# Performance work log

Hardware: AMD Instinct MI355X
Metric: run time of the kernel (lower is better)

## Reference

```python
import jax, jax.numpy as jnp
import numpy as np

D_MODEL = 1024
H = 16
D_K = D_MODEL // H
B, S = 2, 2048

def setup_inputs() -> dict:
    key = jax.random.key(0)
    ks = jax.random.split(key, 13)
    scale = 1.0 / np.sqrt(D_MODEL)
    mk = lambda k: jax.random.normal(k, (D_MODEL, D_MODEL), dtype=jnp.float32) * scale
    return {
        'q': jax.random.normal(ks[0], (B, S, D_MODEL), dtype=jnp.float32),
        'k': jax.random.normal(ks[1], (B, S, D_MODEL), dtype=jnp.float32),
        'v': jax.random.normal(ks[2], (B, S, D_MODEL), dtype=jnp.float32),
        'mask': jax.random.randint(ks[3], (B, 1, S, S), 0, 2, dtype=jnp.int32),
        'wq': mk(ks[4]), 'bq': jnp.zeros((D_MODEL,), jnp.float32),
        'wk': mk(ks[5]), 'bk': jnp.zeros((D_MODEL,), jnp.float32),
        'wv': mk(ks[6]), 'bv': jnp.zeros((D_MODEL,), jnp.float32),
        'wo': mk(ks[7]), 'bo': jnp.zeros((D_MODEL,), jnp.float32),
    }

def reference(q, k, v, mask, wq, bq, wk, bk, wv, bv, wo, bo):
    b, s, _ = q.shape
    # linear projections then split heads: [B,S,D] -> [B,H,S,Dk]
    def proj(x, w, bias):
        y = x @ w + bias
        return y.reshape(b, -1, H, D_K).transpose(0, 2, 1, 3)
    Q = proj(q, wq, bq)
    K = proj(k, wk, bk)
    V = proj(v, wv, bv)
    scores = jnp.einsum('bhqd,bhkd->bhqk', Q, K) / jnp.sqrt(jnp.float32(D_K))
    # faithful to source: masked positions are set to 1e-9 (not -inf)
    scores = jnp.where(mask == 0, jnp.float32(1e-9), scores)
    attn = jax.nn.softmax(scores, axis=-1)  # dropout is identity in eval mode
    x = jnp.einsum('bhqk,bhkd->bhqd', attn, V)
    x = x.transpose(0, 2, 1, 3).reshape(b, s, D_MODEL)
    return x @ wo + bo
```

## Files before the change

### kernel.cpp

```cpp
#include <hip/hip_runtime.h>
#include <hip/hip_bf16.h>

#define DM 1024
#define HEADS 16
#define DKK 64
#define BB 2
#define SS 2048
#define MROWS (BB*SS)

typedef __attribute__((ext_vector_type(8))) short bf16x8;
typedef __attribute__((ext_vector_type(4))) float f32x4;
typedef __attribute__((ext_vector_type(2))) unsigned int uv2;
typedef __hip_bfloat16 bf16;

#define SC2 0.1803368801f
#define MB2 1.442695041e-9f

__device__ __forceinline__ void async16(const void* g, void* l) {
    __builtin_amdgcn_global_load_lds((const __attribute__((address_space(1))) void*)g,
                                     (__attribute__((address_space(3))) void*)l, 16, 0, 0);
}

__global__ void prep_kernel(const float* __restrict__ q, const float* __restrict__ k,
                            const float* __restrict__ v,
                            const float* __restrict__ wq, const float* __restrict__ wk,
                            const float* __restrict__ wv, const float* __restrict__ wo,
                            const int* __restrict__ mask,
                            bf16* __restrict__ qkv, bf16* __restrict__ wcat,
                            unsigned long long* __restrict__ bits) {
    __shared__ float tile[32][33];
    const int bid = blockIdx.x;
    const int tid = threadIdx.x;
    if (bid < 12288) {
        const int z = bid >> 12;
        const int i = ((bid & 4095) << 8) + tid;
        const float* src = z == 0 ? q : (z == 1 ? k : v);
        float4 val = ((const float4*)src)[i];
        union { bf16 b[4]; ushort4 u; } cvt;
        cvt.b[0] = __float2bfloat16(val.x);
        cvt.b[1] = __float2bfloat16(val.y);
        cvt.b[2] = __float2bfloat16(val.z);
        cvt.b[3] = __float2bfloat16(val.w);
        ((ushort4*)(qkv + (size_t)z * MROWS * DM))[i] = cvt.u;
    } else if (bid < 12288 + 4096) {
        const int t = bid - 12288;
        const int z = t >> 10;
        const int bx = t & 31, by = (t >> 5) & 31;
        const float* src = z == 0 ? wq : (z == 1 ? wk : (z == 2 ? wv : wo));
        bf16* dst = wcat + ((size_t)z << 20);
        const int tx = tid & 31, ty = tid >> 5;
        const int x = bx * 32 + tx, y0 = by * 32 + ty;
#pragma unroll
        for (int i = 0; i < 32; i += 8)
            tile[ty + i][tx] = src[(size_t)(y0 + i) * DM + x];
        __syncthreads();
        const int nx = by * 32 + tx, ny0 = bx * 32 + ty;
#pragma unroll
        for (int i = 0; i < 32; i += 8)
            dst[(size_t)(ny0 + i) * DM + nx] = __float2bfloat16(tile[tx][ty + i]);
    } else {
        const int i4 = ((bid - 16384) << 8) + tid;
        const int4 m = ((const int4*)mask)[i4];
        unsigned long long vv = (unsigned long long)(
            (m.x != 0 ? 1u : 0u) | (m.y != 0 ? 2u : 0u) |
            (m.z != 0 ? 4u : 0u) | (m.w != 0 ? 8u : 0u));
        vv <<= ((tid & 15) * 4);
        vv |= __shfl_xor(vv, 1);
        vv |= __shfl_xor(vv, 2);
        vv |= __shfl_xor(vv, 4);
        vv |= __shfl_xor(vv, 8);
        if ((tid & 15) == 0) bits[i4 >> 4] = vv;
    }
}

__global__ __launch_bounds__(256) void gemm_qkv(const bf16* __restrict__ qb, const bf16* __restrict__ kb,
                                                const bf16* __restrict__ vb, const bf16* __restrict__ wcat,
                                                const float* __restrict__ bq, const float* __restrict__ bk,
                                                const float* __restrict__ bv,
                                                bf16* __restrict__ Qh, bf16* __restrict__ Kh,
                                                bf16* __restrict__ Vt) {
    __shared__ __align__(16) bf16 lA[128 * 32];
    __shared__ __align__(16) bf16 lB[128 * 32];
    const int seg = blockIdx.x >> 3;
    const bf16* A    = seg == 0 ? qb : (seg == 1 ? kb : vb);
    const bf16* Bt   = wcat + ((size_t)seg << 20);
    const float* bias = seg == 0 ? bq : (seg == 1 ? bk : bv);

    const int tid  = threadIdx.x;
    const int lane = tid & 63;
    const int lm   = lane & 15;
    const int quad = lane >> 4;
    const int w    = tid >> 6;
    const int wm   = w >> 1, wn = w & 1;
    const int m0   = blockIdx.y * 128;
    const int n0   = (blockIdx.x & 7) * 128;
    const int wbase = w << 6;

    f32x4 acc[4][4];
#pragma unroll
    for (int i = 0; i < 4; ++i)
#pragma unroll
        for (int j = 0; j < 4; ++j) acc[i][j] = (f32x4){0.f, 0.f, 0.f, 0.f};

    for (int kt = 0; kt < DM / 32; ++kt) {
#pragma unroll
        for (int r = 0; r < 2; ++r) {
            const int idx = r * 256 + tid;
            const int row = idx >> 2;
            const int kc  = idx & 3;
            async16(A + (size_t)(m0 + row) * DM + kt * 32 + kc * 8,
                    (char*)lA + (size_t)(r * 256 + wbase) * 16);
            async16(Bt + (size_t)(n0 + row) * DM + kt * 32 + kc * 8,
                    (char*)lB + (size_t)(r * 256 + wbase) * 16);
        }
        __syncthreads();
        bf16x8 af[4], bb[4];
#pragma unroll
        for (int mt = 0; mt < 4; ++mt)
            af[mt] = *(const bf16x8*)&lA[(wm * 64 + mt * 16 + lm) * 32 + quad * 8];
#pragma unroll
        for (int nt = 0; nt < 4; ++nt)
            bb[nt] = *(const bf16x8*)&lB[(wn * 64 + nt * 16 + lm) * 32 + quad * 8];
#pragma unroll
        for (int mt = 0; mt < 4; ++mt)
#pragma unroll
            for (int nt = 0; nt < 4; ++nt)
                acc[mt][nt] = __builtin_amdgcn_mfma_f32_16x16x32_bf16(af[mt], bb[nt], acc[mt][nt], 0, 0, 0);
        __syncthreads();
    }

    if (seg < 2) {
        bf16* outQK = seg == 0 ? Qh : Kh;
        const float oscale = (seg == 1) ? SC2 : 1.0f;
#pragma unroll
        for (int mt = 0; mt < 4; ++mt) {
#pragma unroll
            for (int nt = 0; nt < 4; ++nt) {
                const int gcol = n0 + wn * 64 + nt * 16 + lm;
                const float bvv = bias[gcol];
                const int h = gcol >> 6, d = gcol & 63;
#pragma unroll
                for (int r = 0; r < 4; ++r) {
                    const int grow = m0 + wm * 64 + mt * 16 + quad * 4 + r;
                    const int b = grow >> 11, s = grow & 2047;
                    const float val = (acc[mt][nt][r] + bvv) * oscale;
                    outQK[((size_t)(b * HEADS + h) * SS + s) * DKK + d] = __float2bfloat16(val);
                }
            }
        }
    } else {
#pragma unroll
        for (int mt = 0; mt < 4; ++mt) {
#pragma unroll
            for (int nt = 0; nt < 4; ++nt) {
                const int gcol = n0 + wn * 64 + nt * 16 + lm;
                const float bvv = bias[gcol];
                const int h = gcol >> 6, d = gcol & 63;
                const int growb = m0 + wm * 64 + mt * 16 + quad * 4;
                const int b = growb >> 11, s = growb & 2047;
                union { bf16 hh[4]; uint2 u; } pk;
#pragma unroll
                for (int r = 0; r < 4; ++r) pk.hh[r] = __float2bfloat16(acc[mt][nt][r] + bvv);
                *(uint2*)&Vt[((size_t)(b * HEADS + h) * DKK + d) * SS + s] = pk.u;
            }
        }
    }
}

__global__ __launch_bounds__(256) void gemm_out(const bf16* __restrict__ A, const bf16* __restrict__ Bt,
                                                const float* __restrict__ bias, float* __restrict__ outp) {
    __shared__ __align__(16) bf16 lA[128 * 32];
    __shared__ __align__(16) bf16 lB[64 * 32];
    const int tid  = threadIdx.x;
    const int lane = tid & 63;
    const int lm   = lane & 15;
    const int quad = lane >> 4;
    const int w    = tid >> 6;
    const int m0   = blockIdx.y * 128;
    const int n0   = blockIdx.x * 64;
    const int wbase = w << 6;

    f32x4 acc[2][4];
#pragma unroll
    for (int i = 0; i < 2; ++i)
#pragma unroll
        for (int j = 0; j < 4; ++j) acc[i][j] = (f32x4){0.f, 0.f, 0.f, 0.f};

    for (int kt = 0; kt < DM / 32; ++kt) {
#pragma unroll
        for (int r = 0; r < 2; ++r) {
            const int idx = r * 256 + tid;
            const int row = idx >> 2;
            const int kc  = idx & 3;
            async16(A + (size_t)(m0 + row) * DM + kt * 32 + kc * 8,
                    (char*)lA + (size_t)(r * 256 + wbase) * 16);
        }
        {
            const int row = tid >> 2;
            const int kc  = tid & 3;
            async16(Bt + (size_t)(n0 + row) * DM + kt * 32 + kc * 8,
                    (char*)lB + (size_t)(wbase) * 16);
        }
        __syncthreads();
        bf16x8 af[2], bb[4];
#pragma unroll
        for (int mt = 0; mt < 2; ++mt)
            af[mt] = *(const bf16x8*)&lA[(w * 32 + mt * 16 + lm) * 32 + quad * 8];
#pragma unroll
        for (int nt = 0; nt < 4; ++nt)
            bb[nt] = *(const bf16x8*)&lB[(nt * 16 + lm) * 32 + quad * 8];
#pragma unroll
        for (int mt = 0; mt < 2; ++mt)
#pragma unroll
            for (int nt = 0; nt < 4; ++nt)
                acc[mt][nt] = __builtin_amdgcn_mfma_f32_16x16x32_bf16(af[mt], bb[nt], acc[mt][nt], 0, 0, 0);
        __syncthreads();
    }

#pragma unroll
    for (int mt = 0; mt < 2; ++mt)
#pragma unroll
        for (int nt = 0; nt < 4; ++nt) {
            const int gcol = n0 + nt * 16 + lm;
            const float bvv = bias[gcol];
#pragma unroll
            for (int r = 0; r < 4; ++r) {
                const int grow = m0 + w * 32 + mt * 16 + quad * 4 + r;
                outp[(size_t)grow * DM + gcol] = acc[mt][nt][r] + bvv;
            }
        }
}

__global__ __launch_bounds__(512, 4) void attn_kernel(const bf16* __restrict__ Qh, const bf16* __restrict__ Kh,
                                                      const bf16* __restrict__ Vt,
                                                      const unsigned long long* __restrict__ mbits,
                                                      bf16* __restrict__ ctx) {
    __shared__ __align__(16) char smem[34816];
    bf16* ldsKb = (bf16*)smem;
    bf16* ldsVb = (bf16*)(smem + 16384);
    float* oshare = (float*)smem;
    float* lshare = (float*)(smem + 33792);

    const int tid  = threadIdx.x;
    const int lane = tid & 63;
    const int lm   = lane & 15;
    const int quad = lane >> 4;
    const int w    = tid >> 6;
    const int qg   = w & 3;
    const int kh   = w >> 2;
    const int bh   = blockIdx.y;
    const int b    = bh >> 4;
    const int h    = bh & 15;
    const int q0   = blockIdx.x * 128;
    const int qrow0 = q0 + qg * 32 + lm;

    const int x0 = quad ^ (lm & 7);
    const int x1 = x0 ^ 4;
    const int xh = kh ? x1 : x0;

    const int srow = tid >> 3;
    const int sw   = (tid & 7) ^ (srow & 7);
    const bf16* pK = Kh + (size_t)bh * SS * DKK + (size_t)srow * DKK + sw * 8;
    const bf16* pV = Vt + (size_t)bh * DKK * SS + (size_t)srow * SS + sw * 8;
    char* dK[2] = { (char*)smem + (size_t)tid * 16, (char*)smem + 8192 + (size_t)tid * 16 };
    char* dV[2] = { (char*)smem + 16384 + (size_t)tid * 16, (char*)smem + 24576 + (size_t)tid * 16 };

    const bf16* qp0 = Qh + ((size_t)bh * SS + qrow0) * DKK;
    bf16x8 aq[2][2];
    aq[0][0] = *(const bf16x8*)(qp0 + quad * 8);
    aq[0][1] = *(const bf16x8*)(qp0 + 32 + quad * 8);
    aq[1][0] = *(const bf16x8*)(qp0 + 16 * DKK + quad * 8);
    aq[1][1] = *(const bf16x8*)(qp0 + 16 * DKK + 32 + quad * 8);

    const unsigned long long* pm0 = mbits + ((size_t)b * SS + qrow0) * (SS / 64);
    const unsigned long long* pm1 = pm0 + 16 * (SS / 64);

    f32x4 o[2][4];
#pragma unroll
    for (int i = 0; i < 2; ++i)
#pragma unroll
        for (int j = 0; j < 4; ++j) o[i][j] = (f32x4){0.f, 0.f, 0.f, 0.f};
    float lsum[2] = {0.f, 0.f};

    async16(pK, dK[0]);
    async16(pV, dV[0]);
    __syncthreads();

    const int nkt = SS / 64;
    const int mshift = kh * 32 + quad * 4;

    auto body = [&](int it, int cur) {
        const unsigned long long mw0 = pm0[it];
        const unsigned long long mw1 = pm1[it];
        if (it + 1 < nkt) {
            const int nb = cur ^ 1;
            async16(pK + (size_t)(it + 1) * 64 * DKK, dK[nb]);
            async16(pV + (size_t)(it + 1) * 64, dV[nb]);
        }
        const bf16* lk = ldsKb + cur * 4096;
        const bf16* lv = ldsVb + cur * 4096;

        f32x4 sc[2][2];
#pragma unroll
        for (int mtl = 0; mtl < 2; ++mtl) {
            const int mt = kh * 2 + mtl;
            const bf16x8 kf0 = *(const bf16x8*)&lk[(mt * 16 + lm) * 64 + x0 * 8];
            const bf16x8 kf1 = *(const bf16x8*)&lk[(mt * 16 + lm) * 64 + x1 * 8];
#pragma unroll
            for (int qb = 0; qb < 2; ++qb) {
                sc[qb][mtl] = (f32x4){0.f, 0.f, 0.f, 0.f};
                sc[qb][mtl] = __builtin_amdgcn_mfma_f32_16x16x32_bf16(kf0, aq[qb][0], sc[qb][mtl], 0, 0, 0);
                sc[qb][mtl] = __builtin_amdgcn_mfma_f32_16x16x32_bf16(kf1, aq[qb][1], sc[qb][mtl], 0, 0, 0);
            }
        }

        bf16x8 pf[2];
#pragma unroll
        for (int qb = 0; qb < 2; ++qb) {
            const unsigned long long mq = (qb ? mw1 : mw0) >> mshift;
            unsigned wds[4];
#pragma unroll
            for (int mtl = 0; mtl < 2; ++mtl) {
                const unsigned mmt = (unsigned)(mq >> (mtl * 16));
#pragma unroll
                for (int pp = 0; pp < 2; ++pp) {
                    union { bf16 hh[2]; unsigned u; } wu;
#pragma unroll
                    for (int j = 0; j < 2; ++j) {
                        const int r = pp * 2 + j;
                        const float sv = ((mmt >> r) & 1u) ? sc[qb][mtl][r] : MB2;
                        const float p = __builtin_amdgcn_exp2f(sv);
                        lsum[qb] += p;
                        wu.hh[j] = __float2bfloat16(p);
                    }
                    wds[mtl * 2 + pp] = wu.u;
                }
            }
            const uv2 s1 = __builtin_amdgcn_permlane32_swap(wds[0], wds[2], false, false);
            const uv2 s2 = __builtin_amdgcn_permlane16_swap(s1.x, s1.y, false, false);
            const uv2 s3 = __builtin_amdgcn_permlane32_swap(wds[1], wds[3], false, false);
            const uv2 s4 = __builtin_amdgcn_permlane16_swap(s3.x, s3.y, false, false);
            union { unsigned u[4]; bf16x8 v; } pfu;
            pfu.u[0] = s2.x; pfu.u[1] = s4.x; pfu.u[2] = s2.y; pfu.u[3] = s4.y;
            pf[qb] = pfu.v;
        }

#pragma unroll
        for (int mt = 0; mt < 4; ++mt) {
            const bf16x8 vf = *(const bf16x8*)&lv[(mt * 16 + lm) * 64 + xh * 8];
            o[0][mt] = __builtin_amdgcn_mfma_f32_16x16x32_bf16(vf, pf[0], o[0][mt], 0, 0, 0);
            o[1][mt] = __builtin_amdgcn_mfma_f32_16x16x32_bf16(vf, pf[1], o[1][mt], 0, 0, 0);
        }
        __syncthreads();
    };

    for (int it = 0; it < nkt; it += 2) {
        body(it, 0);
        body(it + 1, 1);
    }

#pragma unroll
    for (int qb = 0; qb < 2; ++qb) {
        lsum[qb] += __shfl_xor(lsum[qb], 16);
        lsum[qb] += __shfl_xor(lsum[qb], 32);
    }

    if (kh == 1) {
#pragma unroll
        for (int qb = 0; qb < 2; ++qb)
#pragma unroll
            for (int mt = 0; mt < 4; ++mt)
                *(f32x4*)&oshare[(size_t)(qg * 32 + qb * 16 + lm) * 66 + mt * 16 + quad * 4] = o[qb][mt];
        if (lane < 32) lshare[qg * 32 + lane] = lsum[lane >> 4];
    }
    __syncthreads();
    if (kh == 0) {
#pragma unroll
        for (int qb = 0; qb < 2; ++qb) {
#pragma unroll
            for (int mt = 0; mt < 4; ++mt)
                o[qb][mt] += *(const f32x4*)&oshare[(size_t)(qg * 32 + qb * 16 + lm) * 66 + mt * 16 + quad * 4];
            const float l = lsum[qb] + lshare[qg * 32 + qb * 16 + lm];
            const float rl = 1.0f / l;
            bf16* crow = ctx + ((size_t)b * SS + qrow0 + qb * 16) * DM + h * DKK;
#pragma unroll
            for (int mt = 0; mt < 4; ++mt) {
                union { bf16 hh[4]; uint2 u; } pk;
#pragma unroll
                for (int r = 0; r < 4; ++r) pk.hh[r] = __float2bfloat16(o[qb][mt][r] * rl);
                *(uint2*)&crow[mt * 16 + quad * 4] = pk.u;
            }
        }
    }
}

extern "C" void kernel_launch(void* const* d_in, const int* in_sizes, int n_in,
                              void* d_out, int out_size, void* d_ws, size_t ws_size,
                              hipStream_t stream) {
    const float* q  = (const float*)d_in[0];
    const float* k  = (const float*)d_in[1];
    const float* v  = (const float*)d_in[2];
    const int* mask = (const int*)d_in[3];
    const float* wq = (const float*)d_in[4];
    const float* bq = (const float*)d_in[5];
    const float* wk = (const float*)d_in[6];
    const float* bk = (const float*)d_in[7];
    const float* wv = (const float*)d_in[8];
    const float* bv = (const float*)d_in[9];
    const float* wo = (const float*)d_in[10];
    const float* bo = (const float*)d_in[11];

    const size_t MB = 1ull << 20;
    char* ws = (char*)d_ws;
    bf16* qkv  = (bf16*)(ws + 0 * MB);
    bf16* wcat = (bf16*)(ws + 24 * MB);
    bf16* wot  = (bf16*)(ws + 30 * MB);
    bf16* Qh   = (bf16*)(ws + 32 * MB);
    bf16* Kh   = (bf16*)(ws + 40 * MB);
    bf16* Vt   = (bf16*)(ws + 48 * MB);
    bf16* ctx  = (bf16*)(ws + 56 * MB);
    unsigned long long* mbits = (unsigned long long*)(ws + 64 * MB);

    prep_kernel<<<24576, 256, 0, stream>>>(q, k, v, wq, wk, wv, wo, mask, qkv, wcat, mbits);

    gemm_qkv<<<dim3(24, 32), 256, 0, stream>>>(qkv, qkv + (size_t)MROWS * DM, qkv + 2 * (size_t)MROWS * DM,
                                               wcat, bq, bk, bv, Qh, Kh, Vt);

    attn_kernel<<<dim3(SS / 128, BB * HEADS), 512, 0, stream>>>(Qh, Kh, Vt, mbits, ctx);

    gemm_out<<<dim3(DM / 64, MROWS / 128), 256, 0, stream>>>(ctx, wot, bo, (float*)d_out);
}
```

Measured before the change: 277.3 us.

## Load K/V fragments directly from global memory in smaller attention blocks

Removes the LDS double-buffered async staging of K and V tiles and the per-tile block barriers. Each wave now reads its K and V MFMA fragments straight from global memory. Blocks shrink from 8 waves covering 128 queries to 2 waves covering 32 queries, with the grid reordered so blocks of the same head run close together. This trades LDS traffic and synchronisation for four times as many global reads of K/V, which now rely on L2/L1 cache hits, and it drops explicit prefetch so load latency is hidden only by occupancy.

```diff
diff --git a/kernel.cpp b/kernel.cpp
--- a/kernel.cpp
+++ b/kernel.cpp
@@ -231,39 +231,26 @@
         }
 }
 
-__global__ __launch_bounds__(512, 4) void attn_kernel(const bf16* __restrict__ Qh, const bf16* __restrict__ Kh,
+__global__ __launch_bounds__(128, 4) void attn_kernel(const bf16* __restrict__ Qh, const bf16* __restrict__ Kh,
                                                       const bf16* __restrict__ Vt,
                                                       const unsigned long long* __restrict__ mbits,
                                                       bf16* __restrict__ ctx) {
-    __shared__ __align__(16) char smem[34816];
-    bf16* ldsKb = (bf16*)smem;
-    bf16* ldsVb = (bf16*)(smem + 16384);
-    float* oshare = (float*)smem;
-    float* lshare = (float*)(smem + 33792);
+    __shared__ __align__(16) float oshare[32 * 66];
+    __shared__ float lshare[32];
 
     const int tid  = threadIdx.x;
     const int lane = tid & 63;
     const int lm   = lane & 15;
     const int quad = lane >> 4;
-    const int w    = tid >> 6;
-    const int qg   = w & 3;
-    const int kh   = w >> 2;
-    const int bh   = blockIdx.y;
+    const int kh   = tid >> 6;
+    const int bh   = blockIdx.x;
     const int b    = bh >> 4;
     const int h    = bh & 15;
-    const int q0   = blockIdx.x * 128;
-    const int qrow0 = q0 + qg * 32 + lm;
-
-    const int x0 = quad ^ (lm & 7);
-    const int x1 = x0 ^ 4;
-    const int xh = kh ? x1 : x0;
-
-    const int srow = tid >> 3;
-    const int sw   = (tid & 7) ^ (srow & 7);
-    const bf16* pK = Kh + (size_t)bh * SS * DKK + (size_t)srow * DKK + sw * 8;
-    const bf16* pV = Vt + (size_t)bh * DKK * SS + (size_t)srow * SS + sw * 8;
-    char* dK[2] = { (char*)smem + (size_t)tid * 16, (char*)smem + 8192 + (size_t)tid * 16 };
-    char* dV[2] = { (char*)smem + 16384 + (size_t)tid * 16, (char*)smem + 24576 + (size_t)tid * 16 };
+    const int q0   = blockIdx.y * 32;
+    const int qrow0 = q0 + lm;
+
+    const bf16* kbase = Kh + (size_t)bh * SS * DKK;
+    const bf16* vbase = Vt + (size_t)bh * DKK * SS;
 
     const bf16* qp0 = Qh + ((size_t)bh * SS + qrow0) * DKK;
     bf16x8 aq[2][2];
@@ -275,6 +262,13 @@
     const unsigned long long* pm0 = mbits + ((size_t)b * SS + qrow0) * (SS / 64);
     const unsigned long long* pm1 = pm0 + 16 * (SS / 64);
 
+    const bf16* pK0 = kbase + (size_t)((kh * 2 + 0) * 16 + lm) * DKK + quad * 8;
+    const bf16* pK1 = kbase + (size_t)((kh * 2 + 1) * 16 + lm) * DKK + quad * 8;
+    const bf16* pV0 = vbase + (size_t)(0 * 16 + lm) * SS + kh * 32 + quad * 8;
+    const bf16* pV1 = vbase + (size_t)(1 * 16 + lm) * SS + kh * 32 + quad * 8;
+    const bf16* pV2 = vbase + (size_t)(2 * 16 + lm) * SS + kh * 32 + quad * 8;
+    const bf16* pV3 = vbase + (size_t)(3 * 16 + lm) * SS + kh * 32 + quad * 8;
+
     f32x4 o[2][4];
 #pragma unroll
     for (int i = 0; i < 2; ++i)
@@ -282,36 +276,31 @@
         for (int j = 0; j < 4; ++j) o[i][j] = (f32x4){0.f, 0.f, 0.f, 0.f};
     float lsum[2] = {0.f, 0.f};
 
-    async16(pK, dK[0]);
-    async16(pV, dV[0]);
-    __syncthreads();
-
-    const int nkt = SS / 64;
     const int mshift = kh * 32 + quad * 4;
 
-    auto body = [&](int it, int cur) {
+    for (int it = 0; it < SS / 64; ++it) {
         const unsigned long long mw0 = pm0[it];
         const unsigned long long mw1 = pm1[it];
-        if (it + 1 < nkt) {
-            const int nb = cur ^ 1;
-            async16(pK + (size_t)(it + 1) * 64 * DKK, dK[nb]);
-            async16(pV + (size_t)(it + 1) * 64, dV[nb]);
-        }
-        const bf16* lk = ldsKb + cur * 4096;
-        const bf16* lv = ldsVb + cur * 4096;
+        const size_t ko = (size_t)it * 64 * DKK;
+        const int so = it * 64;
+        const bf16x8 kf00 = *(const bf16x8*)(pK0 + ko);
+        const bf16x8 kf01 = *(const bf16x8*)(pK0 + ko + 32);
+        const bf16x8 kf10 = *(const bf16x8*)(pK1 + ko);
+        const bf16x8 kf11 = *(const bf16x8*)(pK1 + ko + 32);
+        const bf16x8 vf0 = *(const bf16x8*)(pV0 + so);
+        const bf16x8 vf1 = *(const bf16x8*)(pV1 + so);
+        const bf16x8 vf2 = *(const bf16x8*)(pV2 + so);
+        const bf16x8 vf3 = *(const bf16x8*)(pV3 + so);
 
         f32x4 sc[2][2];
 #pragma unroll
-        for (int mtl = 0; mtl < 2; ++mtl) {
-            const int mt = kh * 2 + mtl;
-            const bf16x8 kf0 = *(const bf16x8*)&lk[(mt * 16 + lm) * 64 + x0 * 8];
-            const bf16x8 kf1 = *(const bf16x8*)&lk[(mt * 16 + lm) * 64 + x1 * 8];
-#pragma unroll
-            for (int qb = 0; qb < 2; ++qb) {
-                sc[qb][mtl] = (f32x4){0.f, 0.f, 0.f, 0.f};
-                sc[qb][mtl] = __builtin_amdgcn_mfma_f32_16x16x32_bf16(kf0, aq[qb][0], sc[qb][mtl], 0, 0, 0);
-                sc[qb][mtl] = __builtin_amdgcn_mfma_f32_16x16x32_bf16(kf1, aq[qb][1], sc[qb][mtl], 0, 0, 0);
-            }
+        for (int qb = 0; qb < 2; ++qb) {
+            sc[qb][0] = (f32x4){0.f, 0.f, 0.f, 0.f};
+            sc[qb][0] = __builtin_amdgcn_mfma_f32_16x16x32_bf16(kf00, aq[qb][0], sc[qb][0], 0, 0, 0);
+            sc[qb][0] = __builtin_amdgcn_mfma_f32_16x16x32_bf16(kf01, aq[qb][1], sc[qb][0], 0, 0, 0);
+            sc[qb][1] = (f32x4){0.f, 0.f, 0.f, 0.f};
+            sc[qb][1] = __builtin_amdgcn_mfma_f32_16x16x32_bf16(kf10, aq[qb][0], sc[qb][1], 0, 0, 0);
+            sc[qb][1] = __builtin_amdgcn_mfma_f32_16x16x32_bf16(kf11, aq[qb][1], sc[qb][1], 0, 0, 0);
         }
 
         bf16x8 pf[2];
@@ -345,18 +334,14 @@
             pf[qb] = pfu.v;
         }
 
-#pragma unroll
-        for (int mt = 0; mt < 4; ++mt) {
-            const bf16x8 vf = *(const bf16x8*)&lv[(mt * 16 + lm) * 64 + xh * 8];
-            o[0][mt] = __builtin_amdgcn_mfma_f32_16x16x32_bf16(vf, pf[0], o[0][mt], 0, 0, 0);
-            o[1][mt] = __builtin_amdgcn_mfma_f32_16x16x32_bf16(vf, pf[1], o[1][mt], 0, 0, 0);
-        }
-        __syncthreads();
-    };
-
-    for (int it = 0; it < nkt; it += 2) {
-        body(it, 0);
-        body(it + 1, 1);
+        o[0][0] = __builtin_amdgcn_mfma_f32_16x16x32_bf16(vf0, pf[0], o[0][0], 0, 0, 0);
+        o[1][0] = __builtin_amdgcn_mfma_f32_16x16x32_bf16(vf0, pf[1], o[1][0], 0, 0, 0);
+        o[0][1] = __builtin_amdgcn_mfma_f32_16x16x32_bf16(vf1, pf[0], o[0][1], 0, 0, 0);
+        o[1][1] = __builtin_amdgcn_mfma_f32_16x16x32_bf16(vf1, pf[1], o[1][1], 0, 0, 0);
+        o[0][2] = __builtin_amdgcn_mfma_f32_16x16x32_bf16(vf2, pf[0], o[0][2], 0, 0, 0);
+        o[1][2] = __builtin_amdgcn_mfma_f32_16x16x32_bf16(vf2, pf[1], o[1][2], 0, 0, 0);
+        o[0][3] = __builtin_amdgcn_mfma_f32_16x16x32_bf16(vf3, pf[0], o[0][3], 0, 0, 0);
+        o[1][3] = __builtin_amdgcn_mfma_f32_16x16x32_bf16(vf3, pf[1], o[1][3], 0, 0, 0);
     }
 
 #pragma unroll
@@ -370,8 +355,8 @@
         for (int qb = 0; qb < 2; ++qb)
 #pragma unroll
             for (int mt = 0; mt < 4; ++mt)
-                *(f32x4*)&oshare[(size_t)(qg * 32 + qb * 16 + lm) * 66 + mt * 16 + quad * 4] = o[qb][mt];
-        if (lane < 32) lshare[qg * 32 + lane] = lsum[lane >> 4];
+                *(f32x4*)&oshare[(size_t)(qb * 16 + lm) * 66 + mt * 16 + quad * 4] = o[qb][mt];
+        if (lane < 32) lshare[lane] = lsum[lane >> 4];
     }
     __syncthreads();
     if (kh == 0) {
@@ -379,8 +364,8 @@
         for (int qb = 0; qb < 2; ++qb) {
 #pragma unroll
             for (int mt = 0; mt < 4; ++mt)
-                o[qb][mt] += *(const f32x4*)&oshare[(size_t)(qg * 32 + qb * 16 + lm) * 66 + mt * 16 + quad * 4];
-            const float l = lsum[qb] + lshare[qg * 32 + qb * 16 + lm];
+                o[qb][mt] += *(const f32x4*)&oshare[(size_t)(qb * 16 + lm) * 66 + mt * 16 + quad * 4];
+            const float l = lsum[qb] + lshare[qb * 16 + lm];
             const float rl = 1.0f / l;
             bf16* crow = ctx + ((size_t)b * SS + qrow0 + qb * 16) * DM + h * DKK;
 #pragma unroll
@@ -426,7 +411,7 @@
     gemm_qkv<<<dim3(24, 32), 256, 0, stream>>>(qkv, qkv + (size_t)MROWS * DM, qkv + 2 * (size_t)MROWS * DM,
                                                wcat, bq, bk, bv, Qh, Kh, Vt);
 
-    attn_kernel<<<dim3(SS / 128, BB * HEADS), 512, 0, stream>>>(Qh, Kh, Vt, mbits, ctx);
+    attn_kernel<<<dim3(BB * HEADS, SS / 32), 128, 0, stream>>>(Qh, Kh, Vt, mbits, ctx);
 
     gemm_out<<<dim3(DM / 64, MROWS / 128), 256, 0, stream>>>(ctx, wot, bo, (float*)d_out);
 }
```

New measurement: 359.6 us. 1.3x slower.
